# Performance work log

Hardware: AMD Instinct MI355X
Metric: run time of the kernel (lower is better)

The kernel has to match this reference:

```python
import jax, jax.numpy as jnp
import numpy as np

B, NPG, F, H, C, DEG = 64, 1024, 128, 128, 10, 16   # graphs, nodes/graph, feat, hidden, classes, degree
N = B * NPG            # 65536 total nodes
E = N * DEG            # 1048576 total edges
K = 820                # ceil(0.8 * 1024) SAGPooling keep count per graph


def _glorot(key, shape):
    lim = float(np.sqrt(6.0 / (shape[0] + shape[1])))
    return jax.random.uniform(key, shape, jnp.float32, -lim, lim)


def setup_inputs() -> dict:
    key = jax.random.key(0)
    ks = jax.random.split(key, 16)
    # edges: endpoints drawn within the same graph
    gid = jnp.repeat(jnp.arange(B, dtype=jnp.int64), NPG * DEG)
    src = gid * NPG + jax.random.randint(ks[0], (E,), 0, NPG, dtype=jnp.int64)
    dst = gid * NPG + jax.random.randint(ks[1], (E,), 0, NPG, dtype=jnp.int64)
    return {
        "x": jax.random.normal(ks[2], (N, F), jnp.float32),
        "src": src,
        "dst": dst,
        # conv1: GraphConv(F, H)  (lin_rel has bias, lin_root has none)
        "W1_rel": _glorot(ks[3], (F, H)), "b1": jnp.zeros((H,), jnp.float32), "W1_root": _glorot(ks[4], (F, H)),
        # convs[0], convs[1]: GraphConv(H, H)
        "W2_rel": _glorot(ks[5], (H, H)), "b2": jnp.zeros((H,), jnp.float32), "W2_root": _glorot(ks[6], (H, H)),
        "W3_rel": _glorot(ks[7], (H, H)), "b3": jnp.zeros((H,), jnp.float32), "W3_root": _glorot(ks[8], (H, H)),
        # SAGPooling score GNN: GraphConv(H, 1)
        "Ws_rel": _glorot(ks[9], (H, 1)), "bs": jnp.zeros((1,), jnp.float32), "Ws_root": _glorot(ks[10], (H, 1)),
        # MLP head
        "Wl1": _glorot(ks[11], (3 * H, H)), "bl1": jnp.zeros((H,), jnp.float32),
        "Wl2": _glorot(ks[12], (H, C)), "bl2": jnp.zeros((C,), jnp.float32),
    }


def _mean_agg(x, src, dst, emask):
    # scatter-mean of source features onto destinations, honoring edge mask
    msg = x[src] * emask[:, None]                                   # [E, d]
    agg = jax.ops.segment_sum(msg, dst, num_segments=N)             # [N, d]
    deg = jax.ops.segment_sum(emask, dst, num_segments=N)           # [N]
    return agg / jnp.maximum(deg, 1.0)[:, None]


def _gconv(x, src, dst, emask, W_rel, b, W_root):
    # PyG GraphConv: lin_rel(mean_j x_j) + lin_root(x)
    return _mean_agg(x, src, dst, emask) @ W_rel + b + x @ W_root


def _gpool(x, nmask):
    # global_mean_pool over valid nodes of each graph
    xm = (x * nmask[:, None]).reshape(B, NPG, -1).sum(axis=1)       # [B, d]
    cnt = nmask.reshape(B, NPG).sum(axis=1)                          # [B]
    return xm / cnt[:, None]


def reference(x, src, dst,
              W1_rel, b1, W1_root, W2_rel, b2, W2_root, W3_rel, b3, W3_root,
              Ws_rel, bs, Ws_root, Wl1, bl1, Wl2, bl2):
    nmask = jnp.ones((N,), x.dtype)
    emask = jnp.ones((E,), x.dtype)

    x = jax.nn.relu(_gconv(x, src, dst, emask, W1_rel, b1, W1_root))
    xs = [_gpool(x, nmask)]

    # convs[0]
    x = jax.nn.relu(_gconv(x, src, dst, emask, W2_rel, b2, W2_root))
    xs.append(_gpool(x, nmask))

    # SAGPooling (ratio=0.8): score via GraphConv(H,1), topk per graph, gate by tanh(score)
    score = _gconv(x, src, dst, emask, Ws_rel, bs, Ws_root)[:, 0]    # [N]
    score_m = jnp.where(nmask > 0, score, -1e30)
    _, idx = jax.lax.top_k(score_m.reshape(B, NPG), K)               # [B, K]
    nmask = jnp.zeros((B, NPG), x.dtype).at[jnp.arange(B)[:, None], idx].set(1.0).reshape(-1)
    x = x * jnp.tanh(score)[:, None] * nmask[:, None]
    emask = emask * nmask[src] * nmask[dst]

    # convs[1]
    x = jax.nn.relu(_gconv(x, src, dst, emask, W3_rel, b3, W3_root))
    xs.append(_gpool(x, nmask))

    h = jnp.concatenate(xs, axis=-1)                                  # [B, 3H] JumpingKnowledge 'cat'
    h = jax.nn.relu(h @ Wl1 + bl1)                                    # dropout: eval mode -> identity
    logits = h @ Wl2 + bl2
    return jax.nn.log_softmax(logits, axis=-1)
```

## Files before the change

### kernel.cpp

```cpp
#include <hip/hip_runtime.h>
#include <hip/hip_bf16.h>

#define NN 65536
#define EE 1048576
#define BG 64
#define NPGC 1024
#define KKEEP 820

typedef unsigned short u16;
typedef unsigned int u32;
typedef __attribute__((ext_vector_type(4))) float f32x4;
typedef __attribute__((ext_vector_type(8))) short bf16x8;

__device__ __forceinline__ float bfu_lo(u32 u) {
    u32 x = u << 16;
    return __builtin_bit_cast(float, x);
}
__device__ __forceinline__ float bfu_hi(u32 u) {
    u32 x = u & 0xffff0000u;
    return __builtin_bit_cast(float, x);
}
__device__ __forceinline__ u16 fbf(float f) {
    __hip_bfloat16 h = __float2bfloat16(f);
    return __builtin_bit_cast(u16, h);
}
__device__ __forceinline__ u32 pack2(float a, float b) {
    return (u32)fbf(a) | ((u32)fbf(b) << 16);
}

__global__ __launch_bounds__(1024) void csr_build_kernel(const int* __restrict__ src,
                                                         const int* __restrict__ dst,
                                                         int* __restrict__ noff,
                                                         int* __restrict__ deg,
                                                         u16* __restrict__ csr16,
                                                         int* __restrict__ nord) {
    __shared__ int hist[NPGC];
    __shared__ int xch[NPGC];
    __shared__ int wsum[16];
    int g = blockIdx.x, t = threadIdx.x;
    int lane = t & 63, wid = t >> 6;
    int ebase = g * 16384;

    int dv[16], sv[16];
#pragma unroll
    for (int j = 0; j < 16; ++j) dv[j] = dst[ebase + (j << 10) + t] & 1023;
#pragma unroll
    for (int j = 0; j < 16; ++j) sv[j] = src[ebase + (j << 10) + t];

    hist[t] = 0;
    __syncthreads();
#pragma unroll
    for (int j = 0; j < 16; ++j) atomicAdd(&hist[dv[j]], 1);
    __syncthreads();

    int d = hist[t];

    int v = d;
#pragma unroll
    for (int s = 1; s < 64; s <<= 1) {
        int u = __shfl_up(v, s, 64);
        if (lane >= s) v += u;
    }
    if (lane == 63) wsum[wid] = v;
    __syncthreads();
    if (t < 16) {
        int w = wsum[t];
#pragma unroll
        for (int s = 1; s < 16; s <<= 1) {
            int u = __shfl_up(w, s, 64);
            if (t >= s) w += u;
        }
        wsum[t] = w;
    }
    __syncthreads();
    int excl = ((wid > 0) ? wsum[wid - 1] : 0) + v - d;

    int node = g * NPGC + t;
    deg[node] = d;
    noff[node] = ebase + excl;
    hist[t] = excl;
    __syncthreads();

#pragma unroll
    for (int j = 0; j < 16; ++j) {
        int p = atomicAdd(&hist[dv[j]], 1);
        csr16[ebase + p] = (u16)(sv[j] & 1023);
    }

    int key = (d << 10) | t;
    for (int k = 2; k <= NPGC; k <<= 1) {
        for (int j = k >> 1; j > 0; j >>= 1) {
            int partner;
            if (j >= 64) {
                xch[t] = key;
                __syncthreads();
                partner = xch[t ^ j];
                __syncthreads();
            } else {
                partner = __shfl_xor(key, j, 64);
            }
            bool up = ((t & k) == 0);
            bool lower = ((t & j) == 0);
            int mn = key < partner ? key : partner;
            int mx = key < partner ? partner : key;
            key = (up == lower) ? mn : mx;
        }
    }
    nord[g * NPGC + t] = key & 1023;
}

__global__ void prep_w_kernel(const float* __restrict__ Wr1, const float* __restrict__ Wo1,
                              const float* __restrict__ Wr2, const float* __restrict__ Wo2,
                              const float* __restrict__ Wr3, const float* __restrict__ Wo3,
                              u16* __restrict__ WT) {
    int l = blockIdx.y;
    const float* Wrel = l == 0 ? Wr1 : (l == 1 ? Wr2 : Wr3);
    const float* Wroot = l == 0 ? Wo1 : (l == 1 ? Wo2 : Wo3);
    int idx = blockIdx.x * 256 + threadIdx.x;
    int col = idx >> 7, k = idx & 127;
    float v = (col < 128) ? Wrel[k * 128 + col] : Wroot[k * 128 + (col - 128)];
    WT[l * 32768 + idx] = fbf(v);
}

template <int MODE>
__global__ __launch_bounds__(256, 2) void gemm_kernel(const u16* __restrict__ Xb,
                                                      const float* __restrict__ Xf,
                                                      const float* __restrict__ gate,
                                                      const u16* __restrict__ WT,
                                                      u16* __restrict__ Y) {
    __shared__ u16 As[128][72];
    __shared__ u16 Bs[128][72];
    int rb = blockIdx.x * 128;
    int cb = blockIdx.y * 128;
    int tid = threadIdx.x;
    int lane = tid & 63, wid = tid >> 6;
    int wr = (wid >> 1) << 6, wc = (wid & 1) << 6;
    int lr = lane & 15, lk = (lane >> 4) << 3;
    f32x4 acc[4][4] = {};

    for (int half = 0; half < 2; ++half) {
        int k0 = half << 6;
        if (half) __syncthreads();
        for (int i = tid; i < 1024; i += 256) {
            int r = i >> 3, c = (i & 7) << 3;
            uint4 av;
            if (MODE == 0) {
                av = *reinterpret_cast<const uint4*>(Xb + (size_t)(rb + r) * 128 + k0 + c);
            } else if (MODE == 1) {
                float4 f0 = *reinterpret_cast<const float4*>(Xf + (size_t)(rb + r) * 128 + k0 + c);
                float4 f1 = *reinterpret_cast<const float4*>(Xf + (size_t)(rb + r) * 128 + k0 + c + 4);
                av.x = pack2(f0.x, f0.y);
                av.y = pack2(f0.z, f0.w);
                av.z = pack2(f1.x, f1.y);
                av.w = pack2(f1.z, f1.w);
            } else {
                float g = gate[rb + r];
                uint4 w = *reinterpret_cast<const uint4*>(Xb + (size_t)(rb + r) * 128 + k0 + c);
                av.x = pack2(bfu_lo(w.x) * g, bfu_hi(w.x) * g);
                av.y = pack2(bfu_lo(w.y) * g, bfu_hi(w.y) * g);
                av.z = pack2(bfu_lo(w.z) * g, bfu_hi(w.z) * g);
                av.w = pack2(bfu_lo(w.w) * g, bfu_hi(w.w) * g);
            }
            *reinterpret_cast<uint4*>(&As[r][c]) = av;
            *reinterpret_cast<uint4*>(&Bs[r][c]) =
                *reinterpret_cast<const uint4*>(WT + (cb + r) * 128 + k0 + c);
        }
        __syncthreads();
        for (int kk = 0; kk < 64; kk += 32) {
            bf16x8 a[4], b[4];
            for (int m = 0; m < 4; ++m)
                a[m] = *reinterpret_cast<const bf16x8*>(&As[wr + m * 16 + lr][kk + lk]);
            for (int n = 0; n < 4; ++n)
                b[n] = *reinterpret_cast<const bf16x8*>(&Bs[wc + n * 16 + lr][kk + lk]);
            for (int m = 0; m < 4; ++m)
                for (int n = 0; n < 4; ++n)
                    acc[m][n] = __builtin_amdgcn_mfma_f32_16x16x32_bf16(a[m], b[n], acc[m][n], 0, 0, 0);
        }
    }
    int orow0 = rb + wr + ((lane >> 4) << 2);
    int ocol0 = cb + wc + (lane & 15);
    for (int m = 0; m < 4; ++m)
        for (int n = 0; n < 4; ++n)
            for (int r = 0; r < 4; ++r)
                Y[(size_t)(orow0 + m * 16 + r) * 256 + ocol0 + n * 16] = fbf(acc[m][n][r]);
}

#define P2IDX(i) ((((i) >> 2) * 20) + 16 + ((i) & 3))
template <int LAYER>
__global__ __launch_bounds__(1024, 4) void agg_kernel(const u16* __restrict__ Y,
                                                      const u16* __restrict__ csr16,
                                                      const int* __restrict__ noff,
                                                      const int* __restrict__ deg,
                                                      const int* __restrict__ nord,
                                                      const float* __restrict__ bias,
                                                      const float* __restrict__ keep,
                                                      const float* __restrict__ cntg,
                                                      u16* __restrict__ outb,
                                                      const float* __restrict__ wsrel,
                                                      const float* __restrict__ wsroot,
                                                      float* __restrict__ srelp,
                                                      float* __restrict__ srootp,
                                                      float* __restrict__ xs,
                                                      int base, float invdenom) {
    __shared__ u32 sst[20480];
    __shared__ u16 csr_s[16384];
    int g = blockIdx.x >> 2, c = blockIdx.x & 3;
    int t = threadIdx.x;
    int nbase = g * NPGC;

    {
        const uint4* sp = reinterpret_cast<const uint4*>(Y + (size_t)(nbase + t) * 256 + c * 32);
        uint4 q0 = sp[0], q1 = sp[1], q2 = sp[2], q3 = sp[3];
        uint4* dp = reinterpret_cast<uint4*>(&sst[t * 20]);
        dp[0] = q0; dp[1] = q1; dp[2] = q2; dp[3] = q3;
    }
    {
        const uint4* cp = reinterpret_cast<const uint4*>(csr16 + ((size_t)g << 14));
        uint4* cd = reinterpret_cast<uint4*>(csr_s);
        cd[t] = cp[t];
        cd[t + 1024] = cp[t + 1024];
    }

    int nloc = nord[nbase + t];
    int node = nbase + nloc;
    int offl = noff[node] - (g << 14), dg = deg[node];
    float ki = 1.f, cnt;
    if (LAYER == 2) {
        ki = keep[node];
        cnt = cntg[node];
    } else {
        cnt = (float)dg;
    }
    __syncthreads();

    float accL[16] = {0.f, 0.f, 0.f, 0.f, 0.f, 0.f, 0.f, 0.f,
                      0.f, 0.f, 0.f, 0.f, 0.f, 0.f, 0.f, 0.f};
    float accH[16] = {0.f, 0.f, 0.f, 0.f, 0.f, 0.f, 0.f, 0.f,
                      0.f, 0.f, 0.f, 0.f, 0.f, 0.f, 0.f, 0.f};
    if (LAYER != 2 || ki != 0.f) {
        int nbr = (dg > 0) ? csr_s[offl] : 0;
        for (int e = 0; e < dg; ++e) {
            int nxt = (e + 1 < dg) ? csr_s[offl + e + 1] : 0;
            const uint4* qp = reinterpret_cast<const uint4*>(&sst[nbr * 20]);
            uint4 q0 = qp[0], q1 = qp[1], q2 = qp[2], q3 = qp[3];
            u32 vv[16] = {q0.x, q0.y, q0.z, q0.w, q1.x, q1.y, q1.z, q1.w,
                          q2.x, q2.y, q2.z, q2.w, q3.x, q3.y, q3.z, q3.w};
#pragma unroll
            for (int fp = 0; fp < 16; ++fp) {
                accL[fp] += bfu_lo(vv[fp]);
                accH[fp] += bfu_hi(vv[fp]);
            }
            nbr = nxt;
        }
    }

    float inv = ki / fmaxf(cnt, 1.f);
    const uint4* rp = reinterpret_cast<const uint4*>(Y + (size_t)node * 256 + 128 + c * 32);
    uint4 r0 = rp[0], r1 = rp[1], r2 = rp[2], r3 = rp[3];
    u32 rr[16] = {r0.x, r0.y, r0.z, r0.w, r1.x, r1.y, r1.z, r1.w,
                  r2.x, r2.y, r2.z, r2.w, r3.x, r3.y, r3.z, r3.w};
    u32 pk[16];
    float pr = 0.f, po = 0.f;
#pragma unroll
    for (int fp = 0; fp < 16; ++fp) {
        float lo = fmaxf(accL[fp] * inv + bias[c * 32 + 2 * fp] + bfu_lo(rr[fp]), 0.f) * ki;
        float hi = fmaxf(accH[fp] * inv + bias[c * 32 + 2 * fp + 1] + bfu_hi(rr[fp]), 0.f) * ki;
        if (LAYER == 1) {
            pr += lo * wsrel[c * 32 + 2 * fp] + hi * wsrel[c * 32 + 2 * fp + 1];
            po += lo * wsroot[c * 32 + 2 * fp] + hi * wsroot[c * 32 + 2 * fp + 1];
        }
        pk[fp] = pack2(lo, hi);
    }
    if (LAYER != 2) {
        uint4* op = reinterpret_cast<uint4*>(outb + (size_t)node * 128 + c * 32);
        uint4 o0 = {pk[0], pk[1], pk[2], pk[3]};
        uint4 o1 = {pk[4], pk[5], pk[6], pk[7]};
        uint4 o2 = {pk[8], pk[9], pk[10], pk[11]};
        uint4 o3 = {pk[12], pk[13], pk[14], pk[15]};
        op[0] = o0; op[1] = o1; op[2] = o2; op[3] = o3;
    }
    if (LAYER == 1) {
        srelp[(size_t)c * NN + node] = pr;
        srootp[(size_t)c * NN + node] = po;
    }

    __syncthreads();
    {
        uint4* dp = reinterpret_cast<uint4*>(&sst[t * 20]);
        uint4 o0 = {pk[0], pk[1], pk[2], pk[3]};
        uint4 o1 = {pk[4], pk[5], pk[6], pk[7]};
        uint4 o2 = {pk[8], pk[9], pk[10], pk[11]};
        uint4 o3 = {pk[12], pk[13], pk[14], pk[15]};
        dp[0] = o0; dp[1] = o1; dp[2] = o2; dp[3] = o3;
    }
    __syncthreads();

    {
        int f = t >> 5, sub = t & 31;
        float s = 0.f;
#pragma unroll 4
        for (int k = 0; k < 32; ++k) {
            u32 v = sst[(sub + 32 * k) * 20 + (f >> 1)];
            s += (f & 1) ? bfu_hi(v) : bfu_lo(v);
        }
        sst[P2IDX(f * 33 + sub)] = __builtin_bit_cast(u32, s);
    }
    __syncthreads();
    if (t < 32) {
        float s = 0.f;
#pragma unroll 4
        for (int sub = 0; sub < 32; ++sub)
            s += __builtin_bit_cast(float, sst[P2IDX(t * 33 + sub)]);
        xs[g * 384 + base + c * 32 + t] = s * invdenom;
    }
}

__global__ __launch_bounds__(1024) void topk_kernel(const float* __restrict__ srelp,
                                                    const float* __restrict__ srootp,
                                                    const float* __restrict__ bs,
                                                    const u16* __restrict__ csr16,
                                                    const int* __restrict__ noff,
                                                    const int* __restrict__ deg,
                                                    float* __restrict__ keep,
                                                    float* __restrict__ gate,
                                                    float* __restrict__ cntg) {
    __shared__ float sc[NPGC];
    __shared__ int si[NPGC];
    __shared__ float ssr[NPGC];
    __shared__ u16 csr_s[16384];
    int g = blockIdx.x, t = threadIdx.x;
    int node = g * NPGC + t;
    {
        const uint4* cp = reinterpret_cast<const uint4*>(csr16 + ((size_t)g << 14));
        uint4* cd = reinterpret_cast<uint4*>(csr_s);
        cd[t] = cp[t];
        cd[t + 1024] = cp[t + 1024];
    }
    ssr[t] = srelp[node] + srelp[NN + node] + srelp[2 * NN + node] + srelp[3 * NN + node];
    float sroot = srootp[node] + srootp[NN + node] + srootp[2 * NN + node] + srootp[3 * NN + node];
    __syncthreads();
    int offl = noff[node] - (g << 14), dg = deg[node];
    float s = 0.f;
    for (int e = 0; e < dg; ++e) s += ssr[csr_s[offl + e]];
    sc[t] = s / fmaxf((float)dg, 1.0f) + bs[0] + sroot;
    si[t] = t;
    __syncthreads();
    for (int k = 2; k <= NPGC; k <<= 1) {
        for (int j = k >> 1; j > 0; j >>= 1) {
            int ixj = t ^ j;
            if (ixj > t) {
                float a = sc[t], b = sc[ixj];
                int ai = si[t], bi = si[ixj];
                bool less = (a > b) || (a == b && ai < bi);
                bool up = ((t & k) == 0);
                if (less != up) { sc[t] = b; sc[ixj] = a; si[t] = bi; si[ixj] = ai; }
            }
            __syncthreads();
        }
    }
    int oloc = si[t];
    float kf = (t < KKEEP) ? 1.f : 0.f;
    keep[g * NPGC + oloc] = kf;
    gate[g * NPGC + oloc] = kf * tanhf(sc[t]);
    ssr[oloc] = kf;
    __syncthreads();
    float cnt = 0.f;
    for (int e = 0; e < dg; ++e) cnt += ssr[csr_s[offl + e]];
    cntg[node] = cnt;
}

__global__ __launch_bounds__(512) void mlp_kernel(const float* __restrict__ xs,
                                                  const float* __restrict__ Wl1,
                                                  const float* __restrict__ bl1,
                                                  const float* __restrict__ Wl2,
                                                  const float* __restrict__ bl2,
                                                  float* __restrict__ out) {
    __shared__ float xsl[384];
    __shared__ float part[4][128];
    __shared__ float wl2s[1280];
    __shared__ float wred[2][10];
    __shared__ float lgs[10];
    int g = blockIdx.x, tid = threadIdx.x;
    int t = tid & 127, kg = tid >> 7;

    for (int i = tid; i < 1280; i += 512) wl2s[i] = Wl2[i];
    if (tid < 384) xsl[tid] = xs[g * 384 + tid];
    __syncthreads();

    float p = 0.f;
    int k0 = kg * 96;
#pragma unroll 8
    for (int k = 0; k < 96; ++k) p += xsl[k0 + k] * Wl1[(k0 + k) * 128 + t];
    part[kg][t] = p;
    __syncthreads();

    if (tid < 128) {
        float h = fmaxf(bl1[t] + part[0][t] + part[1][t] + part[2][t] + part[3][t], 0.f);
        float pc[10];
#pragma unroll
        for (int c = 0; c < 10; ++c) pc[c] = h * wl2s[t * 10 + c];
#pragma unroll
        for (int d = 1; d < 64; d <<= 1) {
#pragma unroll
            for (int c = 0; c < 10; ++c) pc[c] += __shfl_xor(pc[c], d, 64);
        }
        if ((t & 63) == 0) {
#pragma unroll
            for (int c = 0; c < 10; ++c) wred[t >> 6][c] = pc[c];
        }
    }
    __syncthreads();
    if (tid < 10) lgs[tid] = wred[0][tid] + wred[1][tid] + bl2[tid];
    __syncthreads();
    if (tid < 10) {
        float m = lgs[0];
#pragma unroll
        for (int c = 1; c < 10; ++c) m = fmaxf(m, lgs[c]);
        float s = 0.f;
#pragma unroll
        for (int c = 0; c < 10; ++c) s += expf(lgs[c] - m);
        out[g * 10 + tid] = lgs[tid] - m - logf(s);
    }
}

extern "C" void kernel_launch(void* const* d_in, const int* in_sizes, int n_in,
                              void* d_out, int out_size, void* d_ws, size_t ws_size,
                              hipStream_t stream) {
    const float* x       = (const float*)d_in[0];
    const int*   src     = (const int*)d_in[1];
    const int*   dst     = (const int*)d_in[2];
    const float* W1_rel  = (const float*)d_in[3];
    const float* b1      = (const float*)d_in[4];
    const float* W1_root = (const float*)d_in[5];
    const float* W2_rel  = (const float*)d_in[6];
    const float* b2      = (const float*)d_in[7];
    const float* W2_root = (const float*)d_in[8];
    const float* W3_rel  = (const float*)d_in[9];
    const float* b3      = (const float*)d_in[10];
    const float* W3_root = (const float*)d_in[11];
    const float* Ws_rel  = (const float*)d_in[12];
    const float* bs      = (const float*)d_in[13];
    const float* Ws_root = (const float*)d_in[14];
    const float* Wl1     = (const float*)d_in[15];
    const float* bl1     = (const float*)d_in[16];
    const float* Wl2     = (const float*)d_in[17];
    const float* bl2     = (const float*)d_in[18];

    char* ws = (char*)d_ws;
    size_t off = 0;
    auto alloc = [&](size_t bytes) -> void* {
        void* p = ws + off;
        off += (bytes + 255) & ~(size_t)255;
        return p;
    };
    u16*   XB     = (u16*)alloc((size_t)NN * 128 * 2);
    u16*   X2B    = (u16*)alloc((size_t)NN * 128 * 2);
    u16*   YB     = (u16*)alloc((size_t)NN * 256 * 2);
    u16*   WT     = (u16*)alloc(3 * 256 * 128 * 2);
    float* SRELP  = (float*)alloc((size_t)4 * NN * 4);
    float* SROOTP = (float*)alloc((size_t)4 * NN * 4);
    float* GATE   = (float*)alloc(NN * 4);
    float* KEEP   = (float*)alloc(NN * 4);
    float* CNT    = (float*)alloc(NN * 4);
    int*   DEG    = (int*)alloc(NN * 4);
    int*   NOFF   = (int*)alloc(NN * 4);
    int*   NORD   = (int*)alloc(NN * 4);
    u16*   CSR16  = (u16*)alloc((size_t)EE * 2);
    float* XS     = (float*)alloc((size_t)BG * 384 * 4);
    (void)ws_size; (void)n_in; (void)in_sizes; (void)out_size;

    csr_build_kernel<<<BG, 1024, 0, stream>>>(src, dst, NOFF, DEG, CSR16, NORD);

    prep_w_kernel<<<dim3(128, 3), 256, 0, stream>>>(W1_rel, W1_root, W2_rel, W2_root,
                                                    W3_rel, W3_root, WT);

    gemm_kernel<1><<<dim3(NN / 128, 2), 256, 0, stream>>>(nullptr, x, nullptr, WT, YB);
    agg_kernel<0><<<BG * 4, 1024, 0, stream>>>(YB, CSR16, NOFF, DEG, NORD, b1,
                                               nullptr, nullptr, XB,
                                               nullptr, nullptr, nullptr, nullptr,
                                               XS, 0, 1.f / 1024.f);

    gemm_kernel<0><<<dim3(NN / 128, 2), 256, 0, stream>>>(XB, nullptr, nullptr, WT + 32768, YB);
    agg_kernel<1><<<BG * 4, 1024, 0, stream>>>(YB, CSR16, NOFF, DEG, NORD, b2,
                                               nullptr, nullptr, X2B,
                                               Ws_rel, Ws_root, SRELP, SROOTP,
                                               XS, 128, 1.f / 1024.f);

    topk_kernel<<<BG, 1024, 0, stream>>>(SRELP, SROOTP, bs, CSR16, NOFF, DEG, KEEP, GATE, CNT);

    gemm_kernel<2><<<dim3(NN / 128, 2), 256, 0, stream>>>(X2B, nullptr, GATE, WT + 65536, YB);
    agg_kernel<2><<<BG * 4, 1024, 0, stream>>>(YB, CSR16, NOFF, DEG, NORD, b3,
                                               KEEP, CNT, nullptr,
                                               nullptr, nullptr, nullptr, nullptr,
                                               XS, 256, 1.f / (float)KKEEP);

    mlp_kernel<<<BG, 512, 0, stream>>>(XS, Wl1, bl1, Wl2, bl2, (float*)d_out);
}
```

Measured before the change: 169.7 us.

## Add padded per-node neighbor list and split aggregation into two feature halves

The CSR build also writes a padded 32-slot neighbor-index array per node, so the aggregation kernel loads each node's indices with four vector loads instead of staging the whole graph's CSR in shared memory. The aggregation loop runs as two passes over 16-feature halves with a fully unrolled, predicated 32-edge loop, and a global-memory fallback handles degrees above 32. Dropping the CSR shared buffer and halving the accumulator registers is meant to raise occupancy (launch bounds now 1024,8) and cut LDS traffic. The cost is a second pass over the neighbor rows, extra global writes in CSR build, and a 4 MB padded array.

After: 215.7 us. 27.1% more time.

```diff
diff --git a/kernel.cpp b/kernel.cpp
--- a/kernel.cpp
+++ b/kernel.cpp
@@ -33,6 +33,7 @@
                                                          int* __restrict__ noff,
                                                          int* __restrict__ deg,
                                                          u16* __restrict__ csr16,
+                                                         u16* __restrict__ csr16p,
                                                          int* __restrict__ nord) {
     __shared__ int hist[NPGC];
     __shared__ int xch[NPGC];
@@ -79,13 +80,18 @@
     deg[node] = d;
     noff[node] = ebase + excl;
     hist[t] = excl;
+    xch[t] = excl;
     __syncthreads();
 
 #pragma unroll
     for (int j = 0; j < 16; ++j) {
         int p = atomicAdd(&hist[dv[j]], 1);
-        csr16[ebase + p] = (u16)(sv[j] & 1023);
-    }
+        u16 val = (u16)(sv[j] & 1023);
+        csr16[ebase + p] = val;
+        int lp = p - xch[dv[j]];
+        if (lp < 32) csr16p[((size_t)(g * NPGC + dv[j]) << 5) + lp] = val;
+    }
+    __syncthreads();
 
     int key = (d << 10) | t;
     for (int k = 2; k <= NPGC; k <<= 1) {
@@ -187,8 +193,9 @@
 
 #define P2IDX(i) ((((i) >> 2) * 20) + 16 + ((i) & 3))
 template <int LAYER>
-__global__ __launch_bounds__(1024, 4) void agg_kernel(const u16* __restrict__ Y,
+__global__ __launch_bounds__(1024, 8) void agg_kernel(const u16* __restrict__ Y,
                                                       const u16* __restrict__ csr16,
+                                                      const u16* __restrict__ csr16p,
                                                       const int* __restrict__ noff,
                                                       const int* __restrict__ deg,
                                                       const int* __restrict__ nord,
@@ -203,7 +210,6 @@
                                                       float* __restrict__ xs,
                                                       int base, float invdenom) {
     __shared__ u32 sst[20480];
-    __shared__ u16 csr_s[16384];
     int g = blockIdx.x >> 2, c = blockIdx.x & 3;
     int t = threadIdx.x;
     int nbase = g * NPGC;
@@ -214,16 +220,10 @@
         uint4* dp = reinterpret_cast<uint4*>(&sst[t * 20]);
         dp[0] = q0; dp[1] = q1; dp[2] = q2; dp[3] = q3;
     }
-    {
-        const uint4* cp = reinterpret_cast<const uint4*>(csr16 + ((size_t)g << 14));
-        uint4* cd = reinterpret_cast<uint4*>(csr_s);
-        cd[t] = cp[t];
-        cd[t + 1024] = cp[t + 1024];
-    }
 
     int nloc = nord[nbase + t];
     int node = nbase + nloc;
-    int offl = noff[node] - (g << 14), dg = deg[node];
+    int off = noff[node], dg = deg[node];
     float ki = 1.f, cnt;
     if (LAYER == 2) {
         ki = keep[node];
@@ -231,53 +231,77 @@
     } else {
         cnt = (float)dg;
     }
-    __syncthreads();
-
-    float accL[16] = {0.f, 0.f, 0.f, 0.f, 0.f, 0.f, 0.f, 0.f,
-                      0.f, 0.f, 0.f, 0.f, 0.f, 0.f, 0.f, 0.f};
-    float accH[16] = {0.f, 0.f, 0.f, 0.f, 0.f, 0.f, 0.f, 0.f,
-                      0.f, 0.f, 0.f, 0.f, 0.f, 0.f, 0.f, 0.f};
-    if (LAYER != 2 || ki != 0.f) {
-        int nbr = (dg > 0) ? csr_s[offl] : 0;
-        for (int e = 0; e < dg; ++e) {
-            int nxt = (e + 1 < dg) ? csr_s[offl + e + 1] : 0;
-            const uint4* qp = reinterpret_cast<const uint4*>(&sst[nbr * 20]);
-            uint4 q0 = qp[0], q1 = qp[1], q2 = qp[2], q3 = qp[3];
-            u32 vv[16] = {q0.x, q0.y, q0.z, q0.w, q1.x, q1.y, q1.z, q1.w,
-                          q2.x, q2.y, q2.z, q2.w, q3.x, q3.y, q3.z, q3.w};
-#pragma unroll
-            for (int fp = 0; fp < 16; ++fp) {
-                accL[fp] += bfu_lo(vv[fp]);
-                accH[fp] += bfu_hi(vv[fp]);
-            }
-            nbr = nxt;
-        }
-    }
-
+    int dgc = dg < 32 ? dg : 32;
+    bool active = (LAYER != 2) || (ki != 0.f);
     float inv = ki / fmaxf(cnt, 1.f);
-    const uint4* rp = reinterpret_cast<const uint4*>(Y + (size_t)node * 256 + 128 + c * 32);
-    uint4 r0 = rp[0], r1 = rp[1], r2 = rp[2], r3 = rp[3];
-    u32 rr[16] = {r0.x, r0.y, r0.z, r0.w, r1.x, r1.y, r1.z, r1.w,
-                  r2.x, r2.y, r2.z, r2.w, r3.x, r3.y, r3.z, r3.w};
-    u32 pk[16];
+    __syncthreads();
+
+    u32 pkA[8], pkB[8];
     float pr = 0.f, po = 0.f;
-#pragma unroll
-    for (int fp = 0; fp < 16; ++fp) {
-        float lo = fmaxf(accL[fp] * inv + bias[c * 32 + 2 * fp] + bfu_lo(rr[fp]), 0.f) * ki;
-        float hi = fmaxf(accH[fp] * inv + bias[c * 32 + 2 * fp + 1] + bfu_hi(rr[fp]), 0.f) * ki;
-        if (LAYER == 1) {
-            pr += lo * wsrel[c * 32 + 2 * fp] + hi * wsrel[c * 32 + 2 * fp + 1];
-            po += lo * wsroot[c * 32 + 2 * fp] + hi * wsroot[c * 32 + 2 * fp + 1];
-        }
-        pk[fp] = pack2(lo, hi);
-    }
-    if (LAYER != 2) {
-        uint4* op = reinterpret_cast<uint4*>(outb + (size_t)node * 128 + c * 32);
-        uint4 o0 = {pk[0], pk[1], pk[2], pk[3]};
-        uint4 o1 = {pk[4], pk[5], pk[6], pk[7]};
-        uint4 o2 = {pk[8], pk[9], pk[10], pk[11]};
-        uint4 o3 = {pk[12], pk[13], pk[14], pk[15]};
-        op[0] = o0; op[1] = o1; op[2] = o2; op[3] = o3;
+
+#pragma unroll
+    for (int h = 0; h < 2; ++h) {
+        float accL[8] = {0.f, 0.f, 0.f, 0.f, 0.f, 0.f, 0.f, 0.f};
+        float accH[8] = {0.f, 0.f, 0.f, 0.f, 0.f, 0.f, 0.f, 0.f};
+        if (active) {
+            const uint4* ip = reinterpret_cast<const uint4*>(csr16p + ((size_t)node << 5));
+            uint4 i0 = ip[0], i1 = ip[1], i2 = ip[2], i3 = ip[3];
+            u32 wa[16] = {i0.x, i0.y, i0.z, i0.w, i1.x, i1.y, i1.z, i1.w,
+                          i2.x, i2.y, i2.z, i2.w, i3.x, i3.y, i3.z, i3.w};
+#pragma unroll
+            for (int e = 0; e < 32; ++e) {
+                if (e < dgc) {
+                    u32 w = wa[e >> 1];
+                    int nbr = (e & 1) ? (int)(w >> 16) : (int)(w & 0xffffu);
+                    const uint4* qp = reinterpret_cast<const uint4*>(&sst[nbr * 20 + h * 8]);
+                    uint4 q0 = qp[0], q1 = qp[1];
+                    u32 vv[8] = {q0.x, q0.y, q0.z, q0.w, q1.x, q1.y, q1.z, q1.w};
+#pragma unroll
+                    for (int fp = 0; fp < 8; ++fp) {
+                        accL[fp] += bfu_lo(vv[fp]);
+                        accH[fp] += bfu_hi(vv[fp]);
+                    }
+                }
+            }
+            for (int e = 32; e < dg; ++e) {
+                int nbr = csr16[off + e];
+                const uint4* qp = reinterpret_cast<const uint4*>(&sst[nbr * 20 + h * 8]);
+                uint4 q0 = qp[0], q1 = qp[1];
+                u32 vv[8] = {q0.x, q0.y, q0.z, q0.w, q1.x, q1.y, q1.z, q1.w};
+#pragma unroll
+                for (int fp = 0; fp < 8; ++fp) {
+                    accL[fp] += bfu_lo(vv[fp]);
+                    accH[fp] += bfu_hi(vv[fp]);
+                }
+            }
+        }
+        const uint4* rp = reinterpret_cast<const uint4*>(Y + (size_t)node * 256 + 128 + c * 32 + h * 16);
+        uint4 r0 = rp[0], r1 = rp[1];
+        u32 rr[8] = {r0.x, r0.y, r0.z, r0.w, r1.x, r1.y, r1.z, r1.w};
+#pragma unroll
+        for (int fp = 0; fp < 8; ++fp) {
+            int fb = c * 32 + h * 16 + 2 * fp;
+            float lo = fmaxf(accL[fp] * inv + bias[fb] + bfu_lo(rr[fp]), 0.f) * ki;
+            float hi = fmaxf(accH[fp] * inv + bias[fb + 1] + bfu_hi(rr[fp]), 0.f) * ki;
+            if (LAYER == 1) {
+                pr += lo * wsrel[fb] + hi * wsrel[fb + 1];
+                po += lo * wsroot[fb] + hi * wsroot[fb + 1];
+            }
+            if (h == 0) pkA[fp] = pack2(lo, hi);
+            else        pkB[fp] = pack2(lo, hi);
+        }
+        if (LAYER != 2) {
+            uint4* op = reinterpret_cast<uint4*>(outb + (size_t)node * 128 + c * 32 + h * 16);
+            if (h == 0) {
+                uint4 o0 = {pkA[0], pkA[1], pkA[2], pkA[3]};
+                uint4 o1 = {pkA[4], pkA[5], pkA[6], pkA[7]};
+                op[0] = o0; op[1] = o1;
+            } else {
+                uint4 o0 = {pkB[0], pkB[1], pkB[2], pkB[3]};
+                uint4 o1 = {pkB[4], pkB[5], pkB[6], pkB[7]};
+                op[0] = o0; op[1] = o1;
+            }
+        }
     }
     if (LAYER == 1) {
         srelp[(size_t)c * NN + node] = pr;
@@ -287,10 +311,10 @@
     __syncthreads();
     {
         uint4* dp = reinterpret_cast<uint4*>(&sst[t * 20]);
-        uint4 o0 = {pk[0], pk[1], pk[2], pk[3]};
-        uint4 o1 = {pk[4], pk[5], pk[6], pk[7]};
-        uint4 o2 = {pk[8], pk[9], pk[10], pk[11]};
-        uint4 o3 = {pk[12], pk[13], pk[14], pk[15]};
+        uint4 o0 = {pkA[0], pkA[1], pkA[2], pkA[3]};
+        uint4 o1 = {pkA[4], pkA[5], pkA[6], pkA[7]};
+        uint4 o2 = {pkB[0], pkB[1], pkB[2], pkB[3]};
+        uint4 o3 = {pkB[4], pkB[5], pkB[6], pkB[7]};
         dp[0] = o0; dp[1] = o1; dp[2] = o2; dp[3] = o3;
     }
     __syncthreads();
@@ -466,22 +490,23 @@
     int*   NOFF   = (int*)alloc(NN * 4);
     int*   NORD   = (int*)alloc(NN * 4);
     u16*   CSR16  = (u16*)alloc((size_t)EE * 2);
+    u16*   CSR16P = (u16*)alloc((size_t)NN * 32 * 2);
     float* XS     = (float*)alloc((size_t)BG * 384 * 4);
     (void)ws_size; (void)n_in; (void)in_sizes; (void)out_size;
 
-    csr_build_kernel<<<BG, 1024, 0, stream>>>(src, dst, NOFF, DEG, CSR16, NORD);
+    csr_build_kernel<<<BG, 1024, 0, stream>>>(src, dst, NOFF, DEG, CSR16, CSR16P, NORD);
 
     prep_w_kernel<<<dim3(128, 3), 256, 0, stream>>>(W1_rel, W1_root, W2_rel, W2_root,
                                                     W3_rel, W3_root, WT);
 
     gemm_kernel<1><<<dim3(NN / 128, 2), 256, 0, stream>>>(nullptr, x, nullptr, WT, YB);
-    agg_kernel<0><<<BG * 4, 1024, 0, stream>>>(YB, CSR16, NOFF, DEG, NORD, b1,
+    agg_kernel<0><<<BG * 4, 1024, 0, stream>>>(YB, CSR16, CSR16P, NOFF, DEG, NORD, b1,
                                                nullptr, nullptr, XB,
                                                nullptr, nullptr, nullptr, nullptr,
                                                XS, 0, 1.f / 1024.f);
 
     gemm_kernel<0><<<dim3(NN / 128, 2), 256, 0, stream>>>(XB, nullptr, nullptr, WT + 32768, YB);
-    agg_kernel<1><<<BG * 4, 1024, 0, stream>>>(YB, CSR16, NOFF, DEG, NORD, b2,
+    agg_kernel<1><<<BG * 4, 1024, 0, stream>>>(YB, CSR16, CSR16P, NOFF, DEG, NORD, b2,
                                                nullptr, nullptr, X2B,
                                                Ws_rel, Ws_root, SRELP, SROOTP,
                                                XS, 128, 1.f / 1024.f);
@@ -489,7 +514,7 @@
     topk_kernel<<<BG, 1024, 0, stream>>>(SRELP, SROOTP, bs, CSR16, NOFF, DEG, KEEP, GATE, CNT);
 
     gemm_kernel<2><<<dim3(NN / 128, 2), 256, 0, stream>>>(X2B, nullptr, GATE, WT + 65536, YB);
-    agg_kernel<2><<<BG * 4, 1024, 0, stream>>>(YB, CSR16, NOFF, DEG, NORD, b3,
+    agg_kernel<2><<<BG * 4, 1024, 0, stream>>>(YB, CSR16, CSR16P, NOFF, DEG, NORD, b3,
                                                KEEP, CNT, nullptr,
                                                nullptr, nullptr, nullptr, nullptr,
                                                XS, 256, 1.f / (float)KKEEP);
```
